# Optimization experiments

Measured on AMD Instinct MI355X. Metric: run time of the kernel, lower is better.

Reference implementation:

```python
import jax, jax.numpy as jnp
import numpy as np

B, D, OUT = 8192, 1024, 256
H1, H2 = 8, 4
EPS = 1e-5


def setup_inputs() -> dict:
    key = jax.random.key(0)
    ks = jax.random.split(key, 8)
    sc = lambda k, shape: jax.random.normal(k, shape, jnp.float32) * 0.05
    return {
        "x": jax.random.normal(ks[0], (B, D), jnp.float32),
        "W1": sc(ks[1], (D, H1, 1)),      # D diagonal blocks of the masked Linear(D -> 8D)
        "b1": sc(ks[2], (D * H1,)),
        "g1": jnp.ones((D * H1,), jnp.float32),
        "be1": jnp.zeros((D * H1,), jnp.float32),
        "W2": sc(ks[3], (D, H2, H1)),     # D diagonal blocks of the masked Linear(8D -> 4D)
        "b2": sc(ks[4], (D * H2,)),
        "g2": jnp.ones((D * H2,), jnp.float32),
        "be2": jnp.zeros((D * H2,), jnp.float32),
        "Wfc": sc(ks[5], (OUT, D * H2)),
        "bfc": sc(ks[6], (OUT,)),
    }


def _batchnorm(h, g, b):
    # BatchNorm1d in training mode: per-channel batch mean, biased variance
    mu = h.mean(axis=0)
    var = h.var(axis=0)  # ddof=0 (biased), matching torch normalization
    return g * (h - mu) * jax.lax.rsqrt(var + EPS) + b


def reference(x, W1, b1, g1, be1, W2, b2, g2, be2, Wfc, bfc):
    n = x.shape[0]
    # layer 1: per-feature (1 -> H1) block GEMM == masked dense Linear
    h = jnp.einsum("bdi,doi->bdo", x[:, :, None], W1).reshape(n, D * H1)
    h = jax.nn.relu(_batchnorm(h + b1, g1, be1))
    # layer 2: per-feature (H1 -> H2) block GEMM
    h = jnp.einsum("bdi,doi->bdo", h.reshape(n, D, H1), W2).reshape(n, D * H2)
    h = jax.nn.relu(_batchnorm(h + b2, g2, be2))
    # dense output head
    return h @ Wfc.T + bfc
```

## Files before the change

kernel.cpp:

```cpp
#include <hip/hip_runtime.h>

#define EPSV 1e-5f

typedef short bf16x8 __attribute__((ext_vector_type(8)));
typedef float f32x4 __attribute__((ext_vector_type(4)));
typedef const __attribute__((address_space(1))) unsigned int gu32;
typedef __attribute__((address_space(3))) unsigned int lu32;

static __device__ __forceinline__ unsigned short f2b(float f) {
  union { float f; unsigned u; } v; v.f = f;
  return (unsigned short)((v.u + 0x7fffu + ((v.u >> 16) & 1u)) >> 16);
}

__global__ void k_pre(const float* __restrict__ wfc, unsigned short* __restrict__ wb,
                      const float* __restrict__ x, float* __restrict__ ps1) {
  if (blockIdx.x < 512) {
    const int f = blockIdx.x * 256 + threadIdx.x;
    const int l15 = f & 15, quad = (f >> 4) & 3, nb = (f >> 6) & 15, k32b = f >> 10;
    const int n = nb * 16 + l15;
    const int k = k32b * 32 + quad * 8;
    const float4* src = (const float4*)(wfc + (size_t)n * 4096 + k);
    float4 a = src[0], b = src[1];
    ushort4 o0, o1;
    o0.x = f2b(a.x); o0.y = f2b(a.y); o0.z = f2b(a.z); o0.w = f2b(a.w);
    o1.x = f2b(b.x); o1.y = f2b(b.y); o1.z = f2b(b.z); o1.w = f2b(b.w);
    *(ushort4*)(wb + (size_t)f * 8) = o0;
    *(ushort4*)(wb + (size_t)f * 8 + 4) = o1;
  } else {
    const int blk = blockIdx.x - 512;
    const int c = threadIdx.x * 4;
    const int r0 = blk * 32;
    float4 s = {0.f,0.f,0.f,0.f}, q = {0.f,0.f,0.f,0.f};
    for (int g = 0; g < 4; ++g) {
      float4 v[8];
#pragma unroll
      for (int j = 0; j < 8; ++j)
        v[j] = *(const float4*)(x + (size_t)(r0 + g*8 + j) * 1024 + c);
#pragma unroll
      for (int j = 0; j < 8; ++j) {
        s.x += v[j].x; s.y += v[j].y; s.z += v[j].z; s.w += v[j].w;
        q.x = fmaf(v[j].x, v[j].x, q.x); q.y = fmaf(v[j].y, v[j].y, q.y);
        q.z = fmaf(v[j].z, v[j].z, q.z); q.w = fmaf(v[j].w, v[j].w, q.w);
      }
    }
    *(float4*)(ps1 + (size_t)blk * 2048 + c) = s;
    *(float4*)(ps1 + (size_t)blk * 2048 + 1024 + c) = q;
  }
}

__global__ __launch_bounds__(256) void k_fin1(const float* __restrict__ ps1,
    const float* __restrict__ W1, const float* __restrict__ g1,
    const float* __restrict__ be1, float* __restrict__ pt) {
  __shared__ float redS[8][32], redQ[8][32];
  const int t = threadIdx.x;
  const int d0 = blockIdx.x * 32;
  const int dl = t & 31, slot = t >> 5;
  float s = 0.f, q = 0.f;
  for (int u = 0; u < 32; u += 8) {
#pragma unroll
    for (int w = 0; w < 8; ++w) {
      const size_t base = (size_t)(slot * 32 + u + w) * 2048 + d0 + dl;
      s += ps1[base];
      q += ps1[base + 1024];
    }
  }
  redS[slot][dl] = s; redQ[slot][dl] = q;
  __syncthreads();
  const int dloc = t >> 3, i = t & 7;
  float xs = 0.f, xq = 0.f;
#pragma unroll
  for (int p = 0; p < 8; ++p) { xs += redS[p][dloc]; xq += redQ[p][dloc]; }
  const float inv = 1.f / 8192.f;
  const int d = d0 + dloc;
  const int c = d * 8 + i;
  float mean = xs * inv;
  float var = xq * inv - mean * mean;
  float w = W1[c];
  float s1 = g1[c] * w * rsqrtf(w * w * var + EPSV);
  float t1 = be1[c] - s1 * mean;
  pt[(size_t)d * 52 + i] = s1;
  pt[(size_t)d * 52 + 8 + i] = t1;
}

__global__ __launch_bounds__(256) void k_stats2(const float* __restrict__ x,
    const float* __restrict__ pt, const float* __restrict__ W2,
    float* __restrict__ ps2s, float* __restrict__ ps2q) {
  __shared__ float red[8][32][8];
  const int t = threadIdx.x;
  const int dl = t & 31, slot = t >> 5;
  const int d = blockIdx.x * 32 + dl;
  float s1v[8], t1v[8], w2v[32];
  {
    const f32x4* pq = (const f32x4*)(pt + (size_t)d * 52);
    f32x4 a = pq[0], b = pq[1], c = pq[2], e = pq[3];
#pragma unroll
    for (int j = 0; j < 4; ++j) {
      s1v[j] = a[j]; s1v[4 + j] = b[j];
      t1v[j] = c[j]; t1v[4 + j] = e[j];
    }
  }
  const float4* wp = (const float4*)(W2 + (size_t)d * 32);
#pragma unroll
  for (int i = 0; i < 8; ++i) {
    float4 v = wp[i];
    w2v[i*4+0]=v.x; w2v[i*4+1]=v.y; w2v[i*4+2]=v.z; w2v[i*4+3]=v.w;
  }
  float s[4] = {0.f,0.f,0.f,0.f}, q[4] = {0.f,0.f,0.f,0.f};
  const int b0 = blockIdx.y * 256 + slot * 32;
  for (int r = 0; r < 32; r += 8) {
    float xv[8];
#pragma unroll
    for (int j = 0; j < 8; ++j)
      xv[j] = x[(size_t)(b0 + r + j) * 1024 + d];
#pragma unroll
    for (int j = 0; j < 8; ++j) {
      float a1[8];
#pragma unroll
      for (int i = 0; i < 8; ++i) a1[i] = fmaxf(fmaf(s1v[i], xv[j], t1v[i]), 0.f);
#pragma unroll
      for (int o = 0; o < 4; ++o) {
        float h = 0.f;
#pragma unroll
        for (int i = 0; i < 8; ++i) h = fmaf(a1[i], w2v[o*8+i], h);
        s[o] += h;
        q[o] = fmaf(h, h, q[o]);
      }
    }
  }
#pragma unroll
  for (int j = 0; j < 4; ++j) {
    red[slot][dl][j] = s[j];
    red[slot][dl][4+j] = q[j];
  }
  __syncthreads();
  const int d2l = t >> 3, j = t & 7;
  float v = 0.f;
#pragma unroll
  for (int p = 0; p < 8; ++p) v += red[p][d2l][j];
  const int c2 = (blockIdx.x * 32 + d2l) * 4 + (t & 3);
  if (j < 4) ps2s[(size_t)blockIdx.y * 4096 + c2] = v;
  else       ps2q[(size_t)blockIdx.y * 4096 + c2] = v;
}

__global__ void k_fin2(const float* __restrict__ W2, const float* __restrict__ g2,
                       const float* __restrict__ be2, const float* __restrict__ ps2s,
                       const float* __restrict__ ps2q, float* __restrict__ pt) {
  const int c2 = blockIdx.x * 256 + threadIdx.x;
  const int d = c2 >> 2, o = c2 & 3;
  float sm = 0.f, sq = 0.f;
#pragma unroll
  for (int b = 0; b < 32; ++b) {
    sm += ps2s[(size_t)b * 4096 + c2];
    sq += ps2q[(size_t)b * 4096 + c2];
  }
  const float inv = 1.f / 8192.f;
  float m = sm * inv;
  float var = sq * inv - m * m;
  float s2 = g2[c2] * rsqrtf(var + EPSV);
  float t2 = be2[c2] - s2 * m;
  pt[(size_t)d * 52 + 48 + o] = t2;
#pragma unroll
  for (int i = 0; i < 8; ++i)
    pt[(size_t)d * 52 + 16 + o * 8 + i] = W2[(size_t)d * 32 + o * 8 + i] * s2;
}

__global__ __launch_bounds__(256, 2) void k_gemm(const float* __restrict__ x,
    const float* __restrict__ pt, const unsigned short* __restrict__ wb,
    const float* __restrict__ bfc, float* __restrict__ out,
    float* __restrict__ part, const int use_part) {
  __shared__ __align__(16) unsigned short Bs[2][32 * 512];
  __shared__ __align__(16) unsigned short As[64 * 72];
  __shared__ __align__(16) float Ps[16 * 52];
  const int t = threadIdx.x;
  const int lane = t & 63;
  const int wv = t >> 6;
  const int m0 = blockIdx.x * 64;
  const int kQ = blockIdx.y;
  const int quad = lane >> 4;
  const int l15 = lane & 15;
  const int dloc = t & 15, rowg = t >> 4;
  const int k32q = kQ * 32;

  f32x4 acc[4][4];
#pragma unroll
  for (int mt = 0; mt < 4; ++mt)
#pragma unroll
    for (int nt = 0; nt < 4; ++nt) {
      f32x4 z = {0.f, 0.f, 0.f, 0.f};
      acc[mt][nt] = z;
    }

  float xv[4];

#define STAGE_B(CH, BUF) do {                                               \
    const int k32b0_ = k32q + (CH) * 2;                                     \
    _Pragma("unroll")                                                       \
    for (int j_ = 0; j_ < 8; ++j_) {                                        \
      const int fl_ = j_ * 4 + wv;                                          \
      const int gfrag_ = (k32b0_ + (fl_ >> 4)) * 16 + (fl_ & 15);           \
      const unsigned short* gp_ = wb + ((size_t)gfrag_ * 64 + lane) * 8;    \
      __builtin_amdgcn_global_load_lds((gu32*)gp_,                          \
          (lu32*)&Bs[BUF][fl_ * 512], 16, 0, 0);                            \
    }                                                                       \
  } while (0)

#define STAGE_P(CH) do {                                                    \
    if (t < 208) {                                                          \
      const float* gp_ = pt + (size_t)(kQ * 256 + (CH) * 16) * 52 + t * 4;  \
      __builtin_amdgcn_global_load_lds((gu32*)gp_,                          \
          (lu32*)&Ps[t * 4], 16, 0, 0);                                     \
    }                                                                       \
  } while (0)

#define PRE_X(CH) do {                                                      \
    const int d_ = kQ * 256 + (CH) * 16 + dloc;                             \
    _Pragma("unroll")                                                       \
    for (int r_ = 0; r_ < 4; ++r_)                                          \
      xv[r_] = x[(size_t)(m0 + rowg * 4 + r_) * 1024 + d_];                 \
  } while (0)

#define GEN_A() do {                                                        \
    const f32x4* pq_ = (const f32x4*)&Ps[dloc * 52];                        \
    float pv_[52];                                                          \
    _Pragma("unroll")                                                       \
    for (int i_ = 0; i_ < 13; ++i_) {                                       \
      f32x4 v_ = pq_[i_];                                                   \
      pv_[i_*4+0] = v_[0]; pv_[i_*4+1] = v_[1];                             \
      pv_[i_*4+2] = v_[2]; pv_[i_*4+3] = v_[3];                             \
    }                                                                       \
    _Pragma("unroll")                                                       \
    for (int r_ = 0; r_ < 4; ++r_) {                                        \
      const float xvv_ = xv[r_];                                            \
      float a1_[8];                                                         \
      _Pragma("unroll")                                                     \
      for (int i_ = 0; i_ < 8; ++i_)                                        \
        a1_[i_] = fmaxf(fmaf(pv_[i_], xvv_, pv_[8 + i_]), 0.f);             \
      unsigned short o4_[4];                                                \
      _Pragma("unroll")                                                     \
      for (int o_ = 0; o_ < 4; ++o_) {                                      \
        float h_ = pv_[48 + o_];                                            \
        _Pragma("unroll")                                                   \
        for (int i_ = 0; i_ < 8; ++i_)                                      \
          h_ = fmaf(a1_[i_], pv_[16 + o_ * 8 + i_], h_);                    \
        o4_[o_] = f2b(fmaxf(h_, 0.f));                                      \
      }                                                                     \
      *(ushort4*)&As[(rowg * 4 + r_) * 72 + dloc * 4] =                     \
          make_ushort4(o4_[0], o4_[1], o4_[2], o4_[3]);                     \
    }                                                                       \
  } while (0)

  STAGE_P(0);
  STAGE_B(0, 0);
  PRE_X(0);
  __syncthreads();
  GEN_A();
  __syncthreads();

  for (int chi = 0; chi < 16; ++chi) {
    const int cur = chi & 1;
    if (chi < 15) {
      PRE_X(chi + 1);
      STAGE_P(chi + 1);
    }
#pragma unroll
    for (int kk = 0; kk < 2; ++kk) {
      bf16x8 af[4];
#pragma unroll
      for (int mt = 0; mt < 4; ++mt)
        af[mt] = *(const bf16x8*)&As[(mt * 16 + l15) * 72 + kk * 32 + quad * 8];
#pragma unroll
      for (int nt = 0; nt < 4; ++nt) {
        const int fl = kk * 16 + wv * 4 + nt;
        bf16x8 bfr = *(const bf16x8*)&Bs[cur][fl * 512 + lane * 8];
#pragma unroll
        for (int mt = 0; mt < 4; ++mt)
          acc[mt][nt] = __builtin_amdgcn_mfma_f32_16x16x32_bf16(af[mt], bfr,
                                                                acc[mt][nt], 0, 0, 0);
      }
    }
    __syncthreads();
    if (chi < 15) {
      STAGE_B(chi + 1, cur ^ 1);
      GEN_A();
    }
    __syncthreads();
  }

#undef STAGE_B
#undef STAGE_P
#undef PRE_X
#undef GEN_A

  if (use_part) {
    float* dst = part + (size_t)kQ * (8192 * 256);
#pragma unroll
    for (int nt = 0; nt < 4; ++nt) {
      const int col = wv * 64 + nt * 16 + l15;
#pragma unroll
      for (int mt = 0; mt < 4; ++mt) {
#pragma unroll
        for (int r = 0; r < 4; ++r) {
          const int row = m0 + mt * 16 + quad * 4 + r;
          dst[(size_t)row * 256 + col] = acc[mt][nt][r];
        }
      }
    }
  } else {
#pragma unroll
    for (int nt = 0; nt < 4; ++nt) {
      const int col = wv * 64 + nt * 16 + l15;
      const float bias = (kQ == 0) ? bfc[col] : 0.f;
#pragma unroll
      for (int mt = 0; mt < 4; ++mt) {
#pragma unroll
        for (int r = 0; r < 4; ++r) {
          const int row = m0 + mt * 16 + quad * 4 + r;
          atomicAdd(&out[(size_t)row * 256 + col], acc[mt][nt][r] + bias);
        }
      }
    }
  }
}

__global__ void k_merge(const float* __restrict__ part, const float* __restrict__ bfc,
                        float* __restrict__ out) {
  const size_t i = (size_t)blockIdx.x * 256 + threadIdx.x;
  const size_t SL = (size_t)8192 * 256;
  f32x4 a = ((const f32x4*)part)[i];
  f32x4 b = ((const f32x4*)(part + SL))[i];
  f32x4 c = ((const f32x4*)(part + 2 * SL))[i];
  f32x4 d = ((const f32x4*)(part + 3 * SL))[i];
  const int col = (int)((i * 4) & 255);
  f32x4 bv = *(const f32x4*)(bfc + col);
  ((f32x4*)out)[i] = a + b + c + d + bv;
}

extern "C" void kernel_launch(void* const* d_in, const int* in_sizes, int n_in,
                              void* d_out, int out_size, void* d_ws, size_t ws_size,
                              hipStream_t stream) {
  const float* x   = (const float*)d_in[0];
  const float* W1  = (const float*)d_in[1];
  const float* g1  = (const float*)d_in[3];
  const float* be1 = (const float*)d_in[4];
  const float* W2  = (const float*)d_in[5];
  const float* g2  = (const float*)d_in[7];
  const float* be2 = (const float*)d_in[8];
  const float* Wfc = (const float*)d_in[9];
  const float* bfc = (const float*)d_in[10];
  float* out = (float*)d_out;

  char* ws = (char*)d_ws;
  unsigned short* wb = (unsigned short*)ws;
  float* pt     = (float*)(ws + (2u << 20));
  float* shared = (float*)(ws + (2u << 20) + (256u << 10));
  float* ps1  = shared;
  float* ps2s = shared;
  float* ps2q = shared + 32 * 4096;

  const size_t PART_OFF = (2u << 20) + (256u << 10) + (2u << 20);
  const size_t PART_SZ  = (size_t)4 * 8192 * 256 * sizeof(float);
  float* part = (float*)(ws + PART_OFF);
  const int use_part = (ws_size >= PART_OFF + PART_SZ) ? 1 : 0;

  if (!use_part)
    hipMemsetAsync(d_out, 0, (size_t)out_size * sizeof(float), stream);

  k_pre   <<<dim3(768),    256, 0, stream>>>(Wfc, wb, x, ps1);
  k_fin1  <<<dim3(32),     256, 0, stream>>>(ps1, W1, g1, be1, pt);
  k_stats2<<<dim3(32, 32), 256, 0, stream>>>(x, pt, W2, ps2s, ps2q);
  k_fin2  <<<dim3(16),     256, 0, stream>>>(W2, g2, be2, ps2s, ps2q, pt);
  k_gemm  <<<dim3(128, 4), 256, 0, stream>>>(x, pt, wb, bfc, out, part, use_part);
  if (use_part)
    k_merge<<<dim3(2048),  256, 0, stream>>>(part, bfc, out);
}
```

Baseline: 161.2 us.

## Split GEMM K into 8 slices with 512-thread blocks and 2x4 wave grid

The k_gemm launch grows from 128x4 blocks of 256 threads to 128x8 blocks of 512 threads. Each block now covers 128 features (K) instead of 256, and its 8 waves form a 2x4 grid over the 64x256 output tile, so each wave owns a 32x64 sub-tile. The aim is more concurrent waves to hide latency and fewer accumulator registers per wave. The cost is doubling the split-K partial buffer to 8 slices, which adds global write and merge read traffic in k_merge. When the workspace is too small it falls back to atomics, which then doubles the atomic adds.

```diff
diff --git a/kernel.cpp b/kernel.cpp
--- a/kernel.cpp
+++ b/kernel.cpp
@@ -164,7 +164,7 @@
     pt[(size_t)d * 52 + 16 + o * 8 + i] = W2[(size_t)d * 32 + o * 8 + i] * s2;
 }
 
-__global__ __launch_bounds__(256, 2) void k_gemm(const float* __restrict__ x,
+__global__ __launch_bounds__(512, 4) void k_gemm(const float* __restrict__ x,
     const float* __restrict__ pt, const unsigned short* __restrict__ wb,
     const float* __restrict__ bfc, float* __restrict__ out,
     float* __restrict__ part, const int use_part) {
@@ -174,29 +174,32 @@
   const int t = threadIdx.x;
   const int lane = t & 63;
   const int wv = t >> 6;
+  const int wM = wv >> 2;
+  const int wN = wv & 3;
   const int m0 = blockIdx.x * 64;
   const int kQ = blockIdx.y;
   const int quad = lane >> 4;
   const int l15 = lane & 15;
   const int dloc = t & 15, rowg = t >> 4;
-  const int k32q = kQ * 32;
-
-  f32x4 acc[4][4];
-#pragma unroll
-  for (int mt = 0; mt < 4; ++mt)
+  const int d0 = kQ * 128;
+  const int k32q = kQ * 16;
+
+  f32x4 acc[2][4];
+#pragma unroll
+  for (int mt = 0; mt < 2; ++mt)
 #pragma unroll
     for (int nt = 0; nt < 4; ++nt) {
       f32x4 z = {0.f, 0.f, 0.f, 0.f};
       acc[mt][nt] = z;
     }
 
-  float xv[4];
+  float xv[2];
 
 #define STAGE_B(CH, BUF) do {                                               \
     const int k32b0_ = k32q + (CH) * 2;                                     \
     _Pragma("unroll")                                                       \
-    for (int j_ = 0; j_ < 8; ++j_) {                                        \
-      const int fl_ = j_ * 4 + wv;                                          \
+    for (int j_ = 0; j_ < 4; ++j_) {                                        \
+      const int fl_ = j_ * 8 + wv;                                          \
       const int gfrag_ = (k32b0_ + (fl_ >> 4)) * 16 + (fl_ & 15);           \
       const unsigned short* gp_ = wb + ((size_t)gfrag_ * 64 + lane) * 8;    \
       __builtin_amdgcn_global_load_lds((gu32*)gp_,                          \
@@ -206,17 +209,17 @@
 
 #define STAGE_P(CH) do {                                                    \
     if (t < 208) {                                                          \
-      const float* gp_ = pt + (size_t)(kQ * 256 + (CH) * 16) * 52 + t * 4;  \
+      const float* gp_ = pt + (size_t)(d0 + (CH) * 16) * 52 + t * 4;        \
       __builtin_amdgcn_global_load_lds((gu32*)gp_,                          \
           (lu32*)&Ps[t * 4], 16, 0, 0);                                     \
     }                                                                       \
   } while (0)
 
 #define PRE_X(CH) do {                                                      \
-    const int d_ = kQ * 256 + (CH) * 16 + dloc;                             \
+    const int d_ = d0 + (CH) * 16 + dloc;                                   \
     _Pragma("unroll")                                                       \
-    for (int r_ = 0; r_ < 4; ++r_)                                          \
-      xv[r_] = x[(size_t)(m0 + rowg * 4 + r_) * 1024 + d_];                 \
+    for (int r_ = 0; r_ < 2; ++r_)                                          \
+      xv[r_] = x[(size_t)(m0 + rowg * 2 + r_) * 1024 + d_];                 \
   } while (0)
 
 #define GEN_A() do {                                                        \
@@ -229,7 +232,7 @@
       pv_[i_*4+2] = v_[2]; pv_[i_*4+3] = v_[3];                             \
     }                                                                       \
     _Pragma("unroll")                                                       \
-    for (int r_ = 0; r_ < 4; ++r_) {                                        \
+    for (int r_ = 0; r_ < 2; ++r_) {                                        \
       const float xvv_ = xv[r_];                                            \
       float a1_[8];                                                         \
       _Pragma("unroll")                                                     \
@@ -244,7 +247,7 @@
           h_ = fmaf(a1_[i_], pv_[16 + o_ * 8 + i_], h_);                    \
         o4_[o_] = f2b(fmaxf(h_, 0.f));                                      \
       }                                                                     \
-      *(ushort4*)&As[(rowg * 4 + r_) * 72 + dloc * 4] =                     \
+      *(ushort4*)&As[(rowg * 2 + r_) * 72 + dloc * 4] =                     \
           make_ushort4(o4_[0], o4_[1], o4_[2], o4_[3]);                     \
     }                                                                       \
   } while (0)
@@ -256,30 +259,30 @@
   GEN_A();
   __syncthreads();
 
-  for (int chi = 0; chi < 16; ++chi) {
+  for (int chi = 0; chi < 8; ++chi) {
     const int cur = chi & 1;
-    if (chi < 15) {
+    if (chi < 7) {
       PRE_X(chi + 1);
       STAGE_P(chi + 1);
     }
 #pragma unroll
     for (int kk = 0; kk < 2; ++kk) {
-      bf16x8 af[4];
-#pragma unroll
-      for (int mt = 0; mt < 4; ++mt)
-        af[mt] = *(const bf16x8*)&As[(mt * 16 + l15) * 72 + kk * 32 + quad * 8];
+      bf16x8 af[2];
+#pragma unroll
+      for (int mt = 0; mt < 2; ++mt)
+        af[mt] = *(const bf16x8*)&As[(wM * 32 + mt * 16 + l15) * 72 + kk * 32 + quad * 8];
 #pragma unroll
       for (int nt = 0; nt < 4; ++nt) {
-        const int fl = kk * 16 + wv * 4 + nt;
+        const int fl = kk * 16 + wN * 4 + nt;
         bf16x8 bfr = *(const bf16x8*)&Bs[cur][fl * 512 + lane * 8];
 #pragma unroll
-        for (int mt = 0; mt < 4; ++mt)
+        for (int mt = 0; mt < 2; ++mt)
           acc[mt][nt] = __builtin_amdgcn_mfma_f32_16x16x32_bf16(af[mt], bfr,
                                                                 acc[mt][nt], 0, 0, 0);
       }
     }
     __syncthreads();
-    if (chi < 15) {
+    if (chi < 7) {
       STAGE_B(chi + 1, cur ^ 1);
       GEN_A();
     }
@@ -295,12 +298,12 @@
     float* dst = part + (size_t)kQ * (8192 * 256);
 #pragma unroll
     for (int nt = 0; nt < 4; ++nt) {
-      const int col = wv * 64 + nt * 16 + l15;
-#pragma unroll
-      for (int mt = 0; mt < 4; ++mt) {
+      const int col = wN * 64 + nt * 16 + l15;
+#pragma unroll
+      for (int mt = 0; mt < 2; ++mt) {
 #pragma unroll
         for (int r = 0; r < 4; ++r) {
-          const int row = m0 + mt * 16 + quad * 4 + r;
+          const int row = m0 + wM * 32 + mt * 16 + quad * 4 + r;
           dst[(size_t)row * 256 + col] = acc[mt][nt][r];
         }
       }
@@ -308,13 +311,13 @@
   } else {
 #pragma unroll
     for (int nt = 0; nt < 4; ++nt) {
-      const int col = wv * 64 + nt * 16 + l15;
+      const int col = wN * 64 + nt * 16 + l15;
       const float bias = (kQ == 0) ? bfc[col] : 0.f;
 #pragma unroll
-      for (int mt = 0; mt < 4; ++mt) {
+      for (int mt = 0; mt < 2; ++mt) {
 #pragma unroll
         for (int r = 0; r < 4; ++r) {
-          const int row = m0 + mt * 16 + quad * 4 + r;
+          const int row = m0 + wM * 32 + mt * 16 + quad * 4 + r;
           atomicAdd(&out[(size_t)row * 256 + col], acc[mt][nt][r] + bias);
         }
       }
@@ -326,13 +329,13 @@
                         float* __restrict__ out) {
   const size_t i = (size_t)blockIdx.x * 256 + threadIdx.x;
   const size_t SL = (size_t)8192 * 256;
-  f32x4 a = ((const f32x4*)part)[i];
-  f32x4 b = ((const f32x4*)(part + SL))[i];
-  f32x4 c = ((const f32x4*)(part + 2 * SL))[i];
-  f32x4 d = ((const f32x4*)(part + 3 * SL))[i];
+  f32x4 s = ((const f32x4*)part)[i];
+#pragma unroll
+  for (int k = 1; k < 8; ++k)
+    s += ((const f32x4*)(part + (size_t)k * SL))[i];
   const int col = (int)((i * 4) & 255);
-  f32x4 bv = *(const f32x4*)(bfc + col);
-  ((f32x4*)out)[i] = a + b + c + d + bv;
+  s += *(const f32x4*)(bfc + col);
+  ((f32x4*)out)[i] = s;
 }
 
 extern "C" void kernel_launch(void* const* d_in, const int* in_sizes, int n_in,
@@ -358,7 +361,7 @@
   float* ps2q = shared + 32 * 4096;
 
   const size_t PART_OFF = (2u << 20) + (256u << 10) + (2u << 20);
-  const size_t PART_SZ  = (size_t)4 * 8192 * 256 * sizeof(float);
+  const size_t PART_SZ  = (size_t)8 * 8192 * 256 * sizeof(float);
   float* part = (float*)(ws + PART_OFF);
   const int use_part = (ws_size >= PART_OFF + PART_SZ) ? 1 : 0;
 
@@ -369,7 +372,7 @@
   k_fin1  <<<dim3(32),     256, 0, stream>>>(ps1, W1, g1, be1, pt);
   k_stats2<<<dim3(32, 32), 256, 0, stream>>>(x, pt, W2, ps2s, ps2q);
   k_fin2  <<<dim3(16),     256, 0, stream>>>(W2, g2, be2, ps2s, ps2q, pt);
-  k_gemm  <<<dim3(128, 4), 256, 0, stream>>>(x, pt, wb, bfc, out, part, use_part);
+  k_gemm  <<<dim3(128, 8), 512, 0, stream>>>(x, pt, wb, bfc, out, part, use_part);
   if (use_part)
     k_merge<<<dim3(2048),  256, 0, stream>>>(part, bfc, out);
 }
```

Result: slower. 167.3 us (+3.8%).

## Fuse BN1 finalize into stats2 and merge split-K partials in last GEMM block

Applied to the files above, without the earlier changes.

The layer-1 batchnorm finalize kernel is folded into the stats2 kernel. Each block recomputes the per-feature scale and shift from the ps1 partials into shared memory, and only y==0 blocks write them to pt. The separate k_merge kernel is removed: each k_gemm block bumps a per-row-tile atomic counter, and the last of the four K-split blocks sums the partials plus bias into the output. This drops two launches and a full extra pass, at the cost of redundant finalize work across 32 y-blocks, a memset for the counters, and a tail of merge work in the last-arriving blocks.

```diff
diff --git a/kernel.cpp b/kernel.cpp
--- a/kernel.cpp
+++ b/kernel.cpp
@@ -48,57 +48,56 @@
   }
 }
 
-__global__ __launch_bounds__(256) void k_fin1(const float* __restrict__ ps1,
-    const float* __restrict__ W1, const float* __restrict__ g1,
-    const float* __restrict__ be1, float* __restrict__ pt) {
+__global__ __launch_bounds__(256) void k_stats2(const float* __restrict__ x,
+    const float* __restrict__ ps1, const float* __restrict__ W1,
+    const float* __restrict__ g1, const float* __restrict__ be1,
+    const float* __restrict__ W2, float* __restrict__ ps2s,
+    float* __restrict__ ps2q, float* __restrict__ pt) {
   __shared__ float redS[8][32], redQ[8][32];
-  const int t = threadIdx.x;
-  const int d0 = blockIdx.x * 32;
-  const int dl = t & 31, slot = t >> 5;
-  float s = 0.f, q = 0.f;
-  for (int u = 0; u < 32; u += 8) {
-#pragma unroll
-    for (int w = 0; w < 8; ++w) {
-      const size_t base = (size_t)(slot * 32 + u + w) * 2048 + d0 + dl;
-      s += ps1[base];
-      q += ps1[base + 1024];
-    }
-  }
-  redS[slot][dl] = s; redQ[slot][dl] = q;
-  __syncthreads();
-  const int dloc = t >> 3, i = t & 7;
-  float xs = 0.f, xq = 0.f;
-#pragma unroll
-  for (int p = 0; p < 8; ++p) { xs += redS[p][dloc]; xq += redQ[p][dloc]; }
-  const float inv = 1.f / 8192.f;
-  const int d = d0 + dloc;
-  const int c = d * 8 + i;
-  float mean = xs * inv;
-  float var = xq * inv - mean * mean;
-  float w = W1[c];
-  float s1 = g1[c] * w * rsqrtf(w * w * var + EPSV);
-  float t1 = be1[c] - s1 * mean;
-  pt[(size_t)d * 52 + i] = s1;
-  pt[(size_t)d * 52 + 8 + i] = t1;
-}
-
-__global__ __launch_bounds__(256) void k_stats2(const float* __restrict__ x,
-    const float* __restrict__ pt, const float* __restrict__ W2,
-    float* __restrict__ ps2s, float* __restrict__ ps2q) {
+  __shared__ float sb[32][9], tb[32][9];
   __shared__ float red[8][32][8];
   const int t = threadIdx.x;
   const int dl = t & 31, slot = t >> 5;
-  const int d = blockIdx.x * 32 + dl;
+  const int d0 = blockIdx.x * 32;
+
+  {
+    float s = 0.f, q = 0.f;
+    for (int u = 0; u < 32; u += 8) {
+#pragma unroll
+      for (int w = 0; w < 8; ++w) {
+        const size_t base = (size_t)(slot * 32 + u + w) * 2048 + d0 + dl;
+        s += ps1[base];
+        q += ps1[base + 1024];
+      }
+    }
+    redS[slot][dl] = s; redQ[slot][dl] = q;
+  }
+  __syncthreads();
+  {
+    const int dloc = t >> 3, i = t & 7;
+    float xs = 0.f, xq = 0.f;
+#pragma unroll
+    for (int p = 0; p < 8; ++p) { xs += redS[p][dloc]; xq += redQ[p][dloc]; }
+    const float inv = 1.f / 8192.f;
+    const int d = d0 + dloc;
+    const int c = d * 8 + i;
+    float mean = xs * inv;
+    float var = xq * inv - mean * mean;
+    float w = W1[c];
+    float s1 = g1[c] * w * rsqrtf(w * w * var + EPSV);
+    float t1 = be1[c] - s1 * mean;
+    sb[dloc][i] = s1; tb[dloc][i] = t1;
+    if (blockIdx.y == 0) {
+      pt[(size_t)d * 52 + i] = s1;
+      pt[(size_t)d * 52 + 8 + i] = t1;
+    }
+  }
+  __syncthreads();
+
+  const int d = d0 + dl;
   float s1v[8], t1v[8], w2v[32];
-  {
-    const f32x4* pq = (const f32x4*)(pt + (size_t)d * 52);
-    f32x4 a = pq[0], b = pq[1], c = pq[2], e = pq[3];
-#pragma unroll
-    for (int j = 0; j < 4; ++j) {
-      s1v[j] = a[j]; s1v[4 + j] = b[j];
-      t1v[j] = c[j]; t1v[4 + j] = e[j];
-    }
-  }
+#pragma unroll
+  for (int i = 0; i < 8; ++i) { s1v[i] = sb[dl][i]; t1v[i] = tb[dl][i]; }
   const float4* wp = (const float4*)(W2 + (size_t)d * 32);
 #pragma unroll
   for (int i = 0; i < 8; ++i) {
@@ -167,10 +166,12 @@
 __global__ __launch_bounds__(256, 2) void k_gemm(const float* __restrict__ x,
     const float* __restrict__ pt, const unsigned short* __restrict__ wb,
     const float* __restrict__ bfc, float* __restrict__ out,
-    float* __restrict__ part, const int use_part) {
+    float* __restrict__ part, unsigned int* __restrict__ cnt,
+    const int use_part) {
   __shared__ __align__(16) unsigned short Bs[2][32 * 512];
   __shared__ __align__(16) unsigned short As[64 * 72];
   __shared__ __align__(16) float Ps[16 * 52];
+  __shared__ int lastf;
   const int t = threadIdx.x;
   const int lane = t & 63;
   const int wv = t >> 6;
@@ -179,6 +180,7 @@
   const int quad = lane >> 4;
   const int l15 = lane & 15;
   const int dloc = t & 15, rowg = t >> 4;
+  const int d0 = kQ * 256;
   const int k32q = kQ * 32;
 
   f32x4 acc[4][4];
@@ -206,14 +208,14 @@
 
 #define STAGE_P(CH) do {                                                    \
     if (t < 208) {                                                          \
-      const float* gp_ = pt + (size_t)(kQ * 256 + (CH) * 16) * 52 + t * 4;  \
+      const float* gp_ = pt + (size_t)(d0 + (CH) * 16) * 52 + t * 4;        \
       __builtin_amdgcn_global_load_lds((gu32*)gp_,                          \
           (lu32*)&Ps[t * 4], 16, 0, 0);                                     \
     }                                                                       \
   } while (0)
 
 #define PRE_X(CH) do {                                                      \
-    const int d_ = kQ * 256 + (CH) * 16 + dloc;                             \
+    const int d_ = d0 + (CH) * 16 + dloc;                                   \
     _Pragma("unroll")                                                       \
     for (int r_ = 0; r_ < 4; ++r_)                                          \
       xv[r_] = x[(size_t)(m0 + rowg * 4 + r_) * 1024 + d_];                 \
@@ -305,6 +307,27 @@
         }
       }
     }
+    __threadfence();
+    __syncthreads();
+    if (t == 0)
+      lastf = (atomicAdd(&cnt[blockIdx.x], 1u) == 3u) ? 1 : 0;
+    __syncthreads();
+    if (lastf) {
+      __threadfence();
+      const size_t SL = (size_t)8192 * 256;
+      const size_t base = (size_t)m0 * 256;
+#pragma unroll
+      for (int k = 0; k < 16; ++k) {
+        const size_t i4 = (size_t)k * 256 + t;
+        f32x4 s = ((const f32x4*)(part + base))[i4];
+        s += ((const f32x4*)(part + SL + base))[i4];
+        s += ((const f32x4*)(part + 2 * SL + base))[i4];
+        s += ((const f32x4*)(part + 3 * SL + base))[i4];
+        const int col = (int)((i4 * 4) & 255);
+        s += *(const f32x4*)(bfc + col);
+        ((f32x4*)(out + base))[i4] = s;
+      }
+    }
   } else {
 #pragma unroll
     for (int nt = 0; nt < 4; ++nt) {
@@ -320,19 +343,6 @@
       }
     }
   }
-}
-
-__global__ void k_merge(const float* __restrict__ part, const float* __restrict__ bfc,
-                        float* __restrict__ out) {
-  const size_t i = (size_t)blockIdx.x * 256 + threadIdx.x;
-  const size_t SL = (size_t)8192 * 256;
-  f32x4 a = ((const f32x4*)part)[i];
-  f32x4 b = ((const f32x4*)(part + SL))[i];
-  f32x4 c = ((const f32x4*)(part + 2 * SL))[i];
-  f32x4 d = ((const f32x4*)(part + 3 * SL))[i];
-  const int col = (int)((i * 4) & 255);
-  f32x4 bv = *(const f32x4*)(bfc + col);
-  ((f32x4*)out)[i] = a + b + c + d + bv;
 }
 
 extern "C" void kernel_launch(void* const* d_in, const int* in_sizes, int n_in,
@@ -351,25 +361,28 @@
 
   char* ws = (char*)d_ws;
   unsigned short* wb = (unsigned short*)ws;
-  float* pt     = (float*)(ws + (2u << 20));
-  float* shared = (float*)(ws + (2u << 20) + (256u << 10));
-  float* ps1  = shared;
-  float* ps2s = shared;
-  float* ps2q = shared + 32 * 4096;
-
-  const size_t PART_OFF = (2u << 20) + (256u << 10) + (2u << 20);
-  const size_t PART_SZ  = (size_t)4 * 8192 * 256 * sizeof(float);
-  float* part = (float*)(ws + PART_OFF);
-  const int use_part = (ws_size >= PART_OFF + PART_SZ) ? 1 : 0;
-
-  if (!use_part)
+  const size_t OFF_PT   = (size_t)(2u << 20);
+  const size_t OFF_PS1  = OFF_PT + (256u << 10);
+  const size_t OFF_PS2  = OFF_PS1 + (2u << 20);
+  const size_t OFF_PART = OFF_PS2 + (1u << 20);
+  const size_t OFF_CNT  = OFF_PART + ((size_t)32 << 20);
+  float* pt   = (float*)(ws + OFF_PT);
+  float* ps1  = (float*)(ws + OFF_PS1);
+  float* ps2s = (float*)(ws + OFF_PS2);
+  float* ps2q = (float*)(ws + OFF_PS2 + (512u << 10));
+  float* part = (float*)(ws + OFF_PART);
+  unsigned int* cnt = (unsigned int*)(ws + OFF_CNT);
+  const int use_part = (ws_size >= OFF_CNT + 512) ? 1 : 0;
+
+  if (use_part)
+    hipMemsetAsync(cnt, 0, 128 * sizeof(unsigned int), stream);
+  else
     hipMemsetAsync(d_out, 0, (size_t)out_size * sizeof(float), stream);
 
   k_pre   <<<dim3(768),    256, 0, stream>>>(Wfc, wb, x, ps1);
-  k_fin1  <<<dim3(32),     256, 0, stream>>>(ps1, W1, g1, be1, pt);
-  k_stats2<<<dim3(32, 32), 256, 0, stream>>>(x, pt, W2, ps2s, ps2q);
+  k_stats2<<<dim3(32, 32), 256, 0, stream>>>(x, ps1, W1, g1, be1, W2,
+                                             ps2s, ps2q, pt);
   k_fin2  <<<dim3(16),     256, 0, stream>>>(W2, g2, be2, ps2s, ps2q, pt);
-  k_gemm  <<<dim3(128, 4), 256, 0, stream>>>(x, pt, wb, bfc, out, part, use_part);
-  if (use_part)
-    k_merge<<<dim3(2048),  256, 0, stream>>>(part, bfc, out);
-}
+  k_gemm  <<<dim3(128, 4), 256, 0, stream>>>(x, pt, wb, bfc, out, part, cnt,
+                                             use_part);
+}
```

After: 236.7 us. 46.8% more time.
